# Optimization experiments

Measured on AMD Instinct MI355X. Metric: run time of the kernel, lower is better.

Reference implementation:

```python
import jax, jax.numpy as jnp
import numpy as np

B, T, D, N, K, H = 2, 2048, 2048, 16, 8, 128
WIN = 1024                      # sliding_window_size
SOFT_CAP = 50.0                 # attn_logits_soft_cap
SCALAR = 0.08838834764831845    # query_pre_attn_scalar = head_dim**-0.5
K_MASK = -2.3819763e+38
ROPE_BASE = 10000.0
ROPE_SCALE = 1.0


def apply_rope(x, positions):
    # x: [B, T, heads, H]; positions: [B, T]
    head_dim = x.shape[-1]
    half = head_dim // 2
    timescale = ROPE_BASE ** (2.0 * jnp.arange(half, dtype=jnp.float32) / head_dim)
    sinusoid = positions[..., None].astype(jnp.float32) / timescale / ROPE_SCALE  # [B,T,half]
    sin = jnp.sin(sinusoid)[:, :, None, :]
    cos = jnp.cos(sinusoid)[:, :, None, :]
    first, second = jnp.split(x, 2, axis=-1)
    return jnp.concatenate(
        [first * cos - second * sin, second * cos + first * sin], axis=-1
    ).astype(x.dtype)


def setup_inputs() -> dict:
    key = jax.random.key(0)
    k0, k1, k2, k3 = jax.random.split(key, 4)
    x = jax.random.normal(k0, (B, T, D), jnp.float32)
    wq = jax.random.normal(k1, (N, D, H), jnp.float32) * (D ** -0.5)
    wkv = jax.random.normal(k2, (2, K, D, H), jnp.float32) * (D ** -0.5)
    wo = jax.random.normal(k3, (N, H, D), jnp.float32) * ((N * H) ** -0.5)
    segment_pos = jnp.broadcast_to(jnp.arange(T, dtype=jnp.int32), (B, T))
    attn_mask = jnp.broadcast_to(jnp.tril(jnp.ones((T, T), dtype=bool)), (B, T, T))  # causal
    return {"x": x, "wq": wq, "wkv": wkv, "wo": wo,
            "segment_pos": segment_pos, "attn_mask": attn_mask}


def reference(x, wq, wkv, wo, segment_pos, attn_mask):
    # --- projections ---
    q = jnp.einsum('BTD,NDH->BTNH', x, wq)          # [B,T,N,H]
    kv = jnp.einsum('BTD,CKDH->CBTKH', x, wkv)      # [2,B,T,K,H]
    k_proj, v_proj = kv[0], kv[1]
    # --- RoPE + query scaling ---
    q = apply_rope(q, segment_pos) * SCALAR
    k_proj = apply_rope(k_proj, segment_pos)
    # --- GQA logits ---
    G = N // K
    qg = q.reshape(B, T, K, G, H)
    logits = jnp.einsum('BTKGH,BSKH->BTKGS', qg, k_proj).reshape(B, T, N, T)
    # --- soft cap ---
    logits = jnp.tanh(logits / SOFT_CAP) * SOFT_CAP
    # --- sliding-window mask combined with causal attn_mask ---
    all_ones = jnp.ones(attn_mask.shape, dtype=attn_mask.dtype)
    sliding_mask = jnp.triu(all_ones, -WIN + 1) * jnp.tril(all_ones, WIN - 1)
    mask = sliding_mask * attn_mask                  # [B,T,S]
    padded_logits = jnp.where(mask[:, :, None, :], logits, K_MASK)
    probs = jax.nn.softmax(padded_logits, axis=-1).astype(k_proj.dtype)
    # --- GQA weighted values ---
    encoded = jnp.einsum('BTKGS,BSKH->BTKGH',
                         probs.reshape(B, T, K, G, T), v_proj).reshape(B, T, N, H)
    # --- output projection ---
    return jnp.einsum('BTNH,NHD->BTD', encoded, wo)
```

## Files before the change

kernel.cpp:

```cpp
#include <hip/hip_runtime.h>
#include <hip/hip_bf16.h>
#include <stdint.h>

#define BDIM 2
#define TDIM 2048
#define DDIM 2048
#define NHEADS 16
#define KVH 8
#define HDIM 128
#define WINSZ 1024
#define BT (BDIM*TDIM)
#define NHD (NHEADS*HDIM)
#define QKVC 4096

typedef unsigned short u16;
typedef __attribute__((ext_vector_type(8))) short bf16x8;
typedef __attribute__((ext_vector_type(4))) float f32x4;

__device__ __forceinline__ u16 f2bf(float f) {
  union { float f; unsigned u; } v; v.f = f;
  unsigned r = v.u + 0x7FFFu + ((v.u >> 16) & 1u);
  return (u16)(r >> 16);
}
__device__ __forceinline__ float bf2f(u16 u) {
  union { unsigned u; float f; } v; v.u = ((unsigned)u) << 16;
  return v.f;
}

__device__ __forceinline__ void gl_lds16(const u16* g, u16* l) {
  __builtin_amdgcn_global_load_lds((const __attribute__((address_space(1))) void*)g,
                                   (__attribute__((address_space(3))) void*)l, 16, 0, 0);
}

__global__ __launch_bounds__(256) void k_prep(const float* __restrict__ x, const float* __restrict__ wq,
                                              const float* __restrict__ wkv, const float* __restrict__ wo,
                                              const int* __restrict__ seg,
                                              u16* __restrict__ x_bf, u16* __restrict__ wt_qkv,
                                              u16* __restrict__ wo_t, float2* __restrict__ tab) {
  const int id = blockIdx.x, tid = threadIdx.x;
  if (id < 8192) {
    __shared__ float tl0[32][33];
    int tx = tid & 31, ty = tid >> 5;
    int r0 = (id & 127) * 32, c0 = (id >> 7) * 32;
    #pragma unroll
    for (int i = 0; i < 4; i++) {
      int r = r0 + tx, c = c0 + ty + i*8;
      const float* sp; size_t off;
      if (r < 2048) { sp = wq; off = (size_t)(r >> 7)*262144u + (size_t)(r & 127); }
      else { int j = r - 2048; sp = wkv; off = (size_t)((j >> 10)*8 + ((j >> 7) & 7))*262144u + (size_t)(j & 127); }
      off += (size_t)c * 128u;
      tl0[tx][ty + i*8] = sp[off];
    }
    __syncthreads();
    #pragma unroll
    for (int i = 0; i < 4; i++) {
      int rl = ty + i*8;
      wt_qkv[(size_t)(r0 + rl)*2048u + (size_t)(c0 + tx)] = f2bf(tl0[rl][tx]);
    }
  } else if (id < 16384) {
    int i = (id - 8192)*256 + tid;
    float4 v = ((const float4*)x)[i];
    ushort4 o;
    o.x = f2bf(v.x); o.y = f2bf(v.y); o.z = f2bf(v.z); o.w = f2bf(v.w);
    ((ushort4*)x_bf)[i] = o;
  } else if (id < 20480) {
    __shared__ float tl1[32][33];
    int id3 = id - 16384;
    int tx = tid & 31, ty = tid >> 5;
    int r0 = (id3 & 63) * 32, c0 = (id3 >> 6) * 32;
    #pragma unroll
    for (int i = 0; i < 4; i++) {
      int r = r0 + tx, c = c0 + ty + i*8;
      tl1[tx][ty + i*8] = wo[(size_t)c * 2048u + (size_t)r];
    }
    __syncthreads();
    #pragma unroll
    for (int i = 0; i < 4; i++) {
      int rl = ty + i*8;
      wo_t[(size_t)(r0 + rl)*2048u + (size_t)(c0 + tx)] = f2bf(tl1[rl][tx]);
    }
  } else {
    int bt = (id - 20480)*4 + (tid >> 6);
    int i = tid & 63;
    int pos = seg[bt];
    float inv_ts = exp2f(-(float)i * (13.287712379549449f/64.0f));
    float ang = (float)pos * inv_ts;
    tab[(size_t)bt*64 + i] = make_float2(cosf(ang), sinf(ang));
  }
}

template<int F32OUT>
__global__ __launch_bounds__(256) void k_gemm(const u16* __restrict__ A, const u16* __restrict__ Bt,
                                              void* __restrict__ Cout, int M, int Ncols, int Kdim, int ldc) {
  __shared__ u16 As[128*64];
  __shared__ u16 Bs[128*64];
  const int tid = threadIdx.x, lane = tid & 63, wave = tid >> 6;
  const int m0 = blockIdx.x * 128, n0 = blockIdx.y * 128;
  const int wr = wave >> 1, wc = wave & 1;
  const int l15 = lane & 15, lg = lane >> 4;
  f32x4 acc[4][4] = {};
  for (int kt = 0; kt < Kdim; kt += 64) {
    __syncthreads();
    #pragma unroll
    for (int i = 0; i < 4; i++) {
      int chb = i*256 + wave*64;
      int ch = chb + lane;
      int r = ch >> 3, cc = ch & 7;
      gl_lds16(A + (size_t)(m0 + r)*Kdim + kt + cc*8, As + chb*8);
      gl_lds16(Bt + (size_t)(n0 + r)*Kdim + kt + cc*8, Bs + chb*8);
    }
    __syncthreads();
    #pragma unroll
    for (int ks = 0; ks < 2; ks++) {
      bf16x8 af[4], bf[4];
      int kk = ks*32 + lg*8;
      #pragma unroll
      for (int mt = 0; mt < 4; mt++) af[mt] = *(const bf16x8*)(As + (wr*64 + mt*16 + l15)*64 + kk);
      #pragma unroll
      for (int nt = 0; nt < 4; nt++) bf[nt] = *(const bf16x8*)(Bs + (wc*64 + nt*16 + l15)*64 + kk);
      #pragma unroll
      for (int mt = 0; mt < 4; mt++)
        #pragma unroll
        for (int nt = 0; nt < 4; nt++)
          acc[mt][nt] = __builtin_amdgcn_mfma_f32_16x16x32_bf16(af[mt], bf[nt], acc[mt][nt], 0, 0, 0);
    }
  }
  #pragma unroll
  for (int mt = 0; mt < 4; mt++) {
    int row = m0 + wr*64 + mt*16 + lg*4;
    #pragma unroll
    for (int nt = 0; nt < 4; nt++) {
      int col = n0 + wc*64 + nt*16 + l15;
      #pragma unroll
      for (int j = 0; j < 4; j++) {
        if (F32OUT) ((float*)Cout)[(size_t)(row + j)*ldc + col] = acc[mt][nt][j];
        else        ((u16*)Cout)[(size_t)(row + j)*ldc + col] = f2bf(acc[mt][nt][j]);
      }
    }
  }
}

template<int F32OUT>
__global__ __launch_bounds__(512, 2) void k_gemm8(const u16* __restrict__ A, const u16* __restrict__ Bt,
                                                  void* __restrict__ Cout, int M, int Ncols, int Kdim, int ldc) {
  __shared__ u16 As[2][256*64];
  __shared__ u16 Bs[2][256*64];
  const int tid = threadIdx.x, lane = tid & 63, wave = tid >> 6;
  const int l15 = lane & 15, lg = lane >> 4;
  const int wm = wave >> 2, wn = wave & 3;
  const int gx = M >> 8, gy = Ncols >> 8;
  const int nwg = gx * gy;
  int bid = blockIdx.x;
  int q = nwg >> 3, r = nwg & 7;
  int xcd = bid & 7, idx = bid >> 3;
  int wg = (xcd < r ? xcd*(q+1) : r*(q+1) + (xcd - r)*q) + idx;
  const int m0 = (wg % gx) * 256, n0 = (wg / gx) * 256;

  const int st_r = tid >> 3;
  const int st_c = (tid & 7) ^ (st_r & 7);

  const u16* Ag = A + (size_t)(m0 + st_r)*Kdim + st_c*8;
  const u16* Bg = Bt + (size_t)(n0 + st_r)*Kdim + st_c*8;

  auto stage = [&](int t, int h) {
    int buf = t & 1;
    if (h < 2) {
      const u16* g = Bg + (size_t)(h*128)*Kdim + t*64;
      u16* d = &Bs[buf][h*8192 + wave*512];
      gl_lds16(g, d);
      gl_lds16(g + (size_t)64*Kdim, d + 4096);
    } else {
      int hh = h - 2;
      const u16* g = Ag + (size_t)(hh*128)*Kdim + t*64;
      u16* d = &As[buf][hh*8192 + wave*512];
      gl_lds16(g, d);
      gl_lds16(g + (size_t)64*Kdim, d + 4096);
    }
  };

  const int aBase = (wm*128 + l15) * 128;
  const int bBase = (wn*64 + l15) * 128;
  const int kx0 = ((lg) ^ (l15 & 7)) << 4;
  const int kx1 = ((4 + lg) ^ (l15 & 7)) << 4;

  f32x4 acc[8][4] = {};
  bf16x8 af[4][2], bfr[4][2];

  stage(0,0); stage(0,1); stage(0,2); stage(0,3);
  asm volatile("s_waitcnt vmcnt(4)" ::: "memory");
  stage(1,0); stage(1,1); stage(1,2);
  asm volatile("s_waitcnt vmcnt(6)" ::: "memory");
  __builtin_amdgcn_s_barrier();

  const int NT = Kdim >> 6;

#define MFMA_Q(MS, NS)                                                          \
  { _Pragma("unroll") for (int mf = 0; mf < 4; mf++)                            \
    _Pragma("unroll") for (int nf = 0; nf < 2; nf++) {                          \
      acc[(MS)+mf][(NS)+nf] = __builtin_amdgcn_mfma_f32_16x16x32_bf16(af[mf][0], bfr[(NS)+nf][0], acc[(MS)+mf][(NS)+nf], 0, 0, 0); \
      acc[(MS)+mf][(NS)+nf] = __builtin_amdgcn_mfma_f32_16x16x32_bf16(af[mf][1], bfr[(NS)+nf][1], acc[(MS)+mf][(NS)+nf], 0, 0, 0); \
  } }

  for (int t = 0; t < NT; ++t) {
    const int cur = t & 1;
    const char* Ab = (const char*)&As[cur][0];
    const char* Bb = (const char*)&Bs[cur][0];
    #pragma unroll
    for (int mf = 0; mf < 4; mf++) {
      af[mf][0] = *(const bf16x8*)(Ab + aBase + mf*2048 + kx0);
      af[mf][1] = *(const bf16x8*)(Ab + aBase + mf*2048 + kx1);
    }
    #pragma unroll
    for (int nf = 0; nf < 2; nf++) {
      bfr[nf][0] = *(const bf16x8*)(Bb + bBase + nf*2048 + kx0);
      bfr[nf][1] = *(const bf16x8*)(Bb + bBase + nf*2048 + kx1);
    }
    if (t + 1 < NT) stage(t+1, 3);
    asm volatile("s_waitcnt lgkmcnt(8)" ::: "memory");
    __builtin_amdgcn_s_barrier();
    asm volatile("" ::: "memory");
    __builtin_amdgcn_s_setprio(1);
    MFMA_Q(0, 0)
    __builtin_amdgcn_s_setprio(0);
    __builtin_amdgcn_s_barrier();
    #pragma unroll
    for (int nf = 2; nf < 4; nf++) {
      bfr[nf][0] = *(const bf16x8*)(Bb + bBase + nf*2048 + kx0);
      bfr[nf][1] = *(const bf16x8*)(Bb + bBase + nf*2048 + kx1);
    }
    __builtin_amdgcn_s_barrier();
    asm volatile("" ::: "memory");
    __builtin_amdgcn_s_setprio(1);
    MFMA_Q(0, 2)
    __builtin_amdgcn_s_setprio(0);
    __builtin_amdgcn_s_barrier();
    #pragma unroll
    for (int mf = 0; mf < 4; mf++) {
      af[mf][0] = *(const bf16x8*)(Ab + aBase + 8192 + mf*2048 + kx0);
      af[mf][1] = *(const bf16x8*)(Ab + aBase + 8192 + mf*2048 + kx1);
    }
    if (t + 2 < NT) { stage(t+2, 0); stage(t+2, 1); }
    __builtin_amdgcn_s_barrier();
    asm volatile("" ::: "memory");
    __builtin_amdgcn_s_setprio(1);
    MFMA_Q(4, 2)
    __builtin_amdgcn_s_setprio(0);
    __builtin_amdgcn_s_barrier();
    if (t + 2 < NT) {
      stage(t+2, 2);
      asm volatile("s_waitcnt vmcnt(6)" ::: "memory");
    } else if (t + 1 < NT) {
      asm volatile("s_waitcnt vmcnt(0)" ::: "memory");
    }
    __builtin_amdgcn_s_barrier();
    asm volatile("" ::: "memory");
    __builtin_amdgcn_s_setprio(1);
    MFMA_Q(4, 0)
    __builtin_amdgcn_s_setprio(0);
    __builtin_amdgcn_s_barrier();
  }
#undef MFMA_Q

  #pragma unroll
  for (int mf = 0; mf < 8; mf++) {
    int row = m0 + wm*128 + mf*16 + lg*4;
    #pragma unroll
    for (int nf = 0; nf < 4; nf++) {
      int col = n0 + wn*64 + nf*16 + l15;
      #pragma unroll
      for (int j = 0; j < 4; j++) {
        if (F32OUT) ((float*)Cout)[(size_t)(row + j)*ldc + col] = acc[mf][nf][j];
        else        ((u16*)Cout)[(size_t)(row + j)*ldc + col] = f2bf(acc[mf][nf][j]);
      }
    }
  }
}

__global__ __launch_bounds__(256) void k_ropevt(u16* __restrict__ qkv, const float2* __restrict__ tab,
                                                u16* __restrict__ vT) {
  const int id = blockIdx.x, tid = threadIdx.x;
  if (id < 4096) {
    if (tid < 192) {
      const int bt = id;
      const int h = tid >> 3, g = tid & 7;
      const int col0 = (h < 16 ? h*128 : 2048 + (h - 16)*128) + g*8;
      const float sc = (h < 16) ? 0.08838834764831845f : 1.0f;
      u16* row = qkv + (size_t)bt*QKVC;
      bf16x8 v1 = *(const bf16x8*)(row + col0);
      bf16x8 v2 = *(const bf16x8*)(row + col0 + 64);
      const float4* t4 = (const float4*)(tab + (size_t)bt*64 + g*8);
      bf16x8 r1, r2;
      #pragma unroll
      for (int i = 0; i < 4; i++) {
        float4 cs2 = t4[i];
        float f0 = bf2f((u16)v1[2*i]),   s0 = bf2f((u16)v2[2*i]);
        float f1 = bf2f((u16)v1[2*i+1]), s1 = bf2f((u16)v2[2*i+1]);
        r1[2*i]   = (short)f2bf((f0*cs2.x - s0*cs2.y)*sc);
        r2[2*i]   = (short)f2bf((s0*cs2.x + f0*cs2.y)*sc);
        r1[2*i+1] = (short)f2bf((f1*cs2.z - s1*cs2.w)*sc);
        r2[2*i+1] = (short)f2bf((s1*cs2.z + f1*cs2.w)*sc);
      }
      *(bf16x8*)(row + col0) = r1;
      *(bf16x8*)(row + col0 + 64) = r2;
    }
  } else {
    __shared__ u16 tl[32][33];
    const int id2 = id - 4096;
    const int tx = tid & 31, ty = tid >> 5;
    const int t0 = (id2 & 63)*32, h0 = ((id2 >> 6) & 3)*32, bk = id2 >> 8;
    const u16* src = qkv + (size_t)(bk >> 3)*TDIM*QKVC + 3072 + (bk & 7)*HDIM;
    #pragma unroll
    for (int i = 0; i < 4; i++)
      tl[ty + i*8][tx] = src[(size_t)(t0 + ty + i*8)*QKVC + h0 + tx];
    __syncthreads();
    u16* dst = vT + (size_t)bk*HDIM*TDIM;
    #pragma unroll
    for (int i = 0; i < 4; i++)
      dst[(size_t)(h0 + ty + i*8)*TDIM + t0 + tx] = tl[tx][ty + i*8];
  }
}

__device__ __forceinline__ void stage_tiles(const u16* __restrict__ kg, const u16* __restrict__ vg,
                                            u16* ldsK, u16* ldsV, int tid) {
  const int w = tid >> 6;
  const int rK = tid >> 4, cK = tid & 15;
  u16* dK = ldsK + w*512;
  gl_lds16(kg + (size_t)rK*QKVC + ((cK ^ (rK & 15)) << 3), dK);
  gl_lds16(kg + (size_t)(rK + 32)*QKVC + ((cK ^ ((rK + 32) & 15)) << 3), dK + 4096);
  const int rV = tid >> 3, cV = tid & 7;
  u16* dV = ldsV + w*512;
  gl_lds16(vg + (size_t)rV*TDIM + ((cV ^ (rV & 7)) << 3), dV);
  gl_lds16(vg + (size_t)(rV + 64)*TDIM + ((cV ^ ((rV + 64) & 7)) << 3), dV + 4096);
}

__global__ __launch_bounds__(512, 4) void k_attn(const u16* __restrict__ qkv, const u16* __restrict__ vT,
                                                 u16* __restrict__ enc) {
  __shared__ u16 Kb[2][64*128];
  __shared__ u16 Vb[2][128*64];
  __shared__ u16 Pl[8][16*64];
  const int tid = threadIdx.x;
  const int lane = tid & 63, wave = tid >> 6;
  const int l15 = lane & 15, lg = lane >> 4;
  const int wg = blockIdx.x;
  const int lin = (wg & 7)*64 + (wg >> 3);
  const int qt = lin & 31, kvh = (lin >> 5) & 7, b = lin >> 8;
  const int n = kvh*2 + (wave >> 2);
  const int t0 = qt * 64;
  const int lo_row = t0 + (wave & 3)*16, hi_row = lo_row + 15;

  bf16x8 qf[4];
  {
    const u16* qb = qkv + (size_t)(b*TDIM + lo_row + l15)*QKVC + n*HDIM + lg*8;
    #pragma unroll
    for (int ks = 0; ks < 4; ks++) qf[ks] = *(const bf16x8*)(qb + ks*32);
  }
  f32x4 o[8] = {};
  f32x4 o_l = {};
  const short one_bf = (short)0x3F80;
  const bf16x8 ones = {one_bf, one_bf, one_bf, one_bf, one_bf, one_bf, one_bf, one_bf};

  const u16* kgb = qkv + (size_t)(b*TDIM)*QKVC + 2048 + kvh*HDIM;
  const u16* vgb = vT + (size_t)(b*KVH + kvh)*HDIM*TDIM;

  const float L0 = 1.4426950408889634f;
  const float L1 = -1.9235933878519513e-4f;
  const float L2 = 3.0777094205631089e-8f;
  const float BIAS = -72.13475204444817f;

  const int s_begin = (t0 >= 1024) ? (t0 - 1024) : 0;
  stage_tiles(kgb + (size_t)s_begin*QKVC, vgb + s_begin, Kb[0], Vb[0], tid);
  int cur = 0;
  for (int s0 = s_begin; s0 <= t0; s0 += 64) {
    if (s0 + 64 <= t0) {
      stage_tiles(kgb + (size_t)(s0 + 64)*QKVC, vgb + (s0 + 64), Kb[cur ^ 1], Vb[cur ^ 1], tid);
      asm volatile("s_waitcnt vmcnt(4)" ::: "memory");
    } else {
      asm volatile("s_waitcnt vmcnt(0)" ::: "memory");
    }
    __builtin_amdgcn_s_barrier();
    __builtin_amdgcn_sched_barrier(0);

    const u16* Kc = Kb[cur];
    const u16* Vc = Vb[cur];
    f32x4 sc4[4];
    #pragma unroll
    for (int c = 0; c < 4; c++) {
      const int cLo = s0 + c*16;
      bool anyLive = (cLo <= hi_row) && (cLo + 15 >= lo_row - (WINSZ - 1));
      bool full    = (cLo + 15 <= lo_row) && (cLo >= hi_row - (WINSZ - 1));
      f32x4 a = {0.f, 0.f, 0.f, 0.f};
      if (anyLive) {
        int krow = c*16 + l15;
        __builtin_amdgcn_s_setprio(1);
        #pragma unroll
        for (int ks = 0; ks < 4; ks++) {
          bf16x8 kf = *(const bf16x8*)(Kc + krow*128 + (((ks*4 + lg) ^ l15) << 3));
          a = __builtin_amdgcn_mfma_f32_16x16x32_bf16(qf[ks], kf, a, 0, 0, 0);
        }
        __builtin_amdgcn_s_setprio(0);
        if (full) {
          #pragma unroll
          for (int j = 0; j < 4; j++) {
            float z = a[j];
            float u = z*z;
            float tt = __builtin_fmaf(u, __builtin_fmaf(u, L2, L1), L0);
            a[j] = exp2f(__builtin_fmaf(z, tt, BIAS));
          }
        } else {
          #pragma unroll
          for (int j = 0; j < 4; j++) {
            int scol = cLo + l15;
            int trow = lo_row + lg*4 + j;
            float z = a[j];
            float u = z*z;
            float tt = __builtin_fmaf(u, __builtin_fmaf(u, L2, L1), L0);
            float p = exp2f(__builtin_fmaf(z, tt, BIAS));
            bool ok = (scol <= trow) && (scol >= trow - (WINSZ - 1));
            a[j] = ok ? p : 0.f;
          }
        }
      }
      sc4[c] = a;
    }
    #pragma unroll
    for (int c = 0; c < 4; c++)
      #pragma unroll
      for (int j = 0; j < 4; j++) {
        int prow = lg*4 + j, pcol = c*16 + l15;
        int off = prow*128 + pcol*2; off ^= (prow & 7) << 4;
        __hip_bfloat16 hb = __float2bfloat16(sc4[c][j]);
        *(u16*)((char*)(&Pl[wave][0]) + off) = *reinterpret_cast<u16*>(&hb);
      }
    __builtin_amdgcn_s_setprio(1);
    #pragma unroll
    for (int ks = 0; ks < 2; ks++) {
      int roff = l15*128 + ks*64 + lg*16; roff ^= (l15 & 7) << 4;
      bf16x8 pf = *(const bf16x8*)((char*)(&Pl[wave][0]) + roff);
      o_l = __builtin_amdgcn_mfma_f32_16x16x32_bf16(pf, ones, o_l, 0, 0, 0);
      #pragma unroll
      for (int ct = 0; ct < 8; ct++) {
        int vrow = ct*16 + l15;
        bf16x8 vf = *(const bf16x8*)(Vc + vrow*64 + (((ks*4 + lg) ^ (l15 & 7)) << 3));
        o[ct] = __builtin_amdgcn_mfma_f32_16x16x32_bf16(pf, vf, o[ct], 0, 0, 0);
      }
    }
    __builtin_amdgcn_s_setprio(0);
    __builtin_amdgcn_s_barrier();
    cur ^= 1;
  }
  #pragma unroll
  for (int j = 0; j < 4; j++) {
    float inv = __fdividef(1.f, o_l[j]);
    int row = lo_row + lg*4 + j;
    u16* eb = enc + (size_t)(b*TDIM + row)*NHD + n*HDIM;
    #pragma unroll
    for (int ct = 0; ct < 8; ct++)
      eb[ct*16 + l15] = f2bf(o[ct][j] * inv);
  }
}

extern "C" void kernel_launch(void* const* d_in, const int* in_sizes, int n_in,
                              void* d_out, int out_size, void* d_ws, size_t ws_size,
                              hipStream_t stream) {
  const float* x   = (const float*)d_in[0];
  const float* wq  = (const float*)d_in[1];
  const float* wkv = (const float*)d_in[2];
  const float* wo  = (const float*)d_in[3];
  const int*   seg = (const int*)d_in[4];
  float* out = (float*)d_out;

  char* ws = (char*)d_ws;
  u16*    x_bf   = (u16*)(ws);
  u16*    wt_qkv = (u16*)(ws + (16u << 20));
  u16*    qkv    = (u16*)(ws + (32u << 20));
  u16*    vT     = (u16*)(ws + (64u << 20));
  u16*    enc    = (u16*)(ws + (72u << 20));
  u16*    wo_t   = (u16*)(ws + (88u << 20));
  float2* tab    = (float2*)(ws + (96u << 20));

  k_prep<<<dim3(21504), 256, 0, stream>>>(x, wq, wkv, wo, seg, x_bf, wt_qkv, wo_t, tab);
  k_gemm8<0><<<dim3((BT/256)*(QKVC/256)), 512, 0, stream>>>(x_bf, wt_qkv, qkv, BT, QKVC, DDIM, QKVC);
  k_ropevt<<<dim3(8192), 256, 0, stream>>>(qkv, tab, vT);
  k_attn<<<dim3(512), 512, 0, stream>>>(qkv, vT, enc);
  k_gemm<1><<<dim3(BT/128, DDIM/128), 256, 0, stream>>>(enc, wo_t, out, BT, DDIM, NHD, DDIM);
}
```

Before: 204.2 us.

## Fuse Q RoPE into attention, single-buffer K/V, remap output GEMM blocks per XCD

Query RoPE and scaling move from the separate rope kernel into the attention kernel's Q-fragment load, so that kernel now only rotates K and transposes V. Attention drops K/V double buffering for a single buffer with synchronous loads, and raises the occupancy hint from 4 to 6 blocks per CU. The tanh soft-cap polynomial loses its highest-order term, and the output GEMM launches a 1D grid remapped so neighbouring tiles land on the same XCD. The changes trade load/compute overlap for lower LDS use and higher occupancy, and the shorter polynomial slightly changes numerics.

```diff
diff --git a/kernel.cpp b/kernel.cpp
--- a/kernel.cpp
+++ b/kernel.cpp
@@ -1,5 +1,4 @@
 #include <hip/hip_runtime.h>
-#include <hip/hip_bf16.h>
 #include <stdint.h>
 
 #define BDIM 2
@@ -95,7 +94,10 @@
   __shared__ u16 As[128*64];
   __shared__ u16 Bs[128*64];
   const int tid = threadIdx.x, lane = tid & 63, wave = tid >> 6;
-  const int m0 = blockIdx.x * 128, n0 = blockIdx.y * 128;
+  const int bid = blockIdx.x;
+  const int xcd = bid & 7, idx = bid >> 3;
+  const int m0 = (((xcd & 3) << 3) + (idx & 7)) * 128;
+  const int n0 = (((xcd >> 2) << 3) + (idx >> 3)) * 128;
   const int wr = wave >> 1, wc = wave & 1;
   const int l15 = lane & 15, lg = lane >> 4;
   f32x4 acc[4][4] = {};
@@ -276,33 +278,23 @@
   }
 }
 
-__global__ __launch_bounds__(256) void k_ropevt(u16* __restrict__ qkv, const float2* __restrict__ tab,
-                                                u16* __restrict__ vT) {
+__global__ __launch_bounds__(256) void k_kvt(u16* __restrict__ qkv, const float2* __restrict__ tab,
+                                             u16* __restrict__ vT) {
   const int id = blockIdx.x, tid = threadIdx.x;
   if (id < 4096) {
-    if (tid < 192) {
-      const int bt = id;
-      const int h = tid >> 3, g = tid & 7;
-      const int col0 = (h < 16 ? h*128 : 2048 + (h - 16)*128) + g*8;
-      const float sc = (h < 16) ? 0.08838834764831845f : 1.0f;
-      u16* row = qkv + (size_t)bt*QKVC;
-      bf16x8 v1 = *(const bf16x8*)(row + col0);
-      bf16x8 v2 = *(const bf16x8*)(row + col0 + 64);
-      const float4* t4 = (const float4*)(tab + (size_t)bt*64 + g*8);
-      bf16x8 r1, r2;
-      #pragma unroll
-      for (int i = 0; i < 4; i++) {
-        float4 cs2 = t4[i];
-        float f0 = bf2f((u16)v1[2*i]),   s0 = bf2f((u16)v2[2*i]);
-        float f1 = bf2f((u16)v1[2*i+1]), s1 = bf2f((u16)v2[2*i+1]);
-        r1[2*i]   = (short)f2bf((f0*cs2.x - s0*cs2.y)*sc);
-        r2[2*i]   = (short)f2bf((s0*cs2.x + f0*cs2.y)*sc);
-        r1[2*i+1] = (short)f2bf((f1*cs2.z - s1*cs2.w)*sc);
-        r2[2*i+1] = (short)f2bf((s1*cs2.z + f1*cs2.w)*sc);
-      }
-      *(bf16x8*)(row + col0) = r1;
-      *(bf16x8*)(row + col0 + 64) = r2;
-    }
+    const int bt = id;
+    const int kh = tid >> 5, ii = (tid & 31) * 2;
+    u16* row = qkv + (size_t)bt*QKVC + 2048 + kh*128 + ii;
+    const float2 c0 = tab[(size_t)bt*64 + ii];
+    const float2 c1 = tab[(size_t)bt*64 + ii + 1];
+    unsigned fu = *(const unsigned*)row;
+    unsigned su = *(const unsigned*)(row + 64);
+    float f0 = bf2f((u16)(fu & 0xffff)), f1 = bf2f((u16)(fu >> 16));
+    float s0 = bf2f((u16)(su & 0xffff)), s1 = bf2f((u16)(su >> 16));
+    unsigned ro = (unsigned)f2bf(f0*c0.x - s0*c0.y) | ((unsigned)f2bf(f1*c1.x - s1*c1.y) << 16);
+    unsigned rs = (unsigned)f2bf(s0*c0.x + f0*c0.y) | ((unsigned)f2bf(s1*c1.x + f1*c1.y) << 16);
+    *(unsigned*)row = ro;
+    *(unsigned*)(row + 64) = rs;
   } else {
     __shared__ u16 tl[32][33];
     const int id2 = id - 4096;
@@ -333,10 +325,10 @@
   gl_lds16(vg + (size_t)(rV + 64)*TDIM + ((cV ^ ((rV + 64) & 7)) << 3), dV + 4096);
 }
 
-__global__ __launch_bounds__(512, 4) void k_attn(const u16* __restrict__ qkv, const u16* __restrict__ vT,
-                                                 u16* __restrict__ enc) {
-  __shared__ u16 Kb[2][64*128];
-  __shared__ u16 Vb[2][128*64];
+__global__ __launch_bounds__(512, 6) void k_attn(const u16* __restrict__ qkv, const u16* __restrict__ vT,
+                                                 const float2* __restrict__ tab, u16* __restrict__ enc) {
+  __shared__ u16 Kb[64*128];
+  __shared__ u16 Vb[128*64];
   __shared__ u16 Pl[8][16*64];
   const int tid = threadIdx.x;
   const int lane = tid & 63, wave = tid >> 6;
@@ -350,9 +342,21 @@
 
   bf16x8 qf[4];
   {
-    const u16* qb = qkv + (size_t)(b*TDIM + lo_row + l15)*QKVC + n*HDIM + lg*8;
+    const int qrow = b*TDIM + lo_row + l15;
+    const u16* qb = qkv + (size_t)qrow*QKVC + n*HDIM + lg*8;
     #pragma unroll
     for (int ks = 0; ks < 4; ks++) qf[ks] = *(const bf16x8*)(qb + ks*32);
+    const float2* trow = tab + (size_t)qrow*64 + lg*8;
+    const float SC = 0.08838834764831845f;
+    #pragma unroll
+    for (int ks = 0; ks < 2; ks++)
+      #pragma unroll
+      for (int e = 0; e < 8; e++) {
+        float2 cs = trow[ks*32 + e];
+        float f = bf2f((u16)qf[ks][e]), s = bf2f((u16)qf[ks+2][e]);
+        qf[ks][e]   = (short)f2bf((f*cs.x - s*cs.y) * SC);
+        qf[ks+2][e] = (short)f2bf((s*cs.x + f*cs.y) * SC);
+      }
   }
   f32x4 o[8] = {};
   f32x4 o_l = {};
@@ -363,25 +367,16 @@
   const u16* vgb = vT + (size_t)(b*KVH + kvh)*HDIM*TDIM;
 
   const float L0 = 1.4426950408889634f;
-  const float L1 = -1.9235933878519513e-4f;
-  const float L2 = 3.0777094205631089e-8f;
+  const float C1L = -1.9235933878519513e-4f;
   const float BIAS = -72.13475204444817f;
 
   const int s_begin = (t0 >= 1024) ? (t0 - 1024) : 0;
-  stage_tiles(kgb + (size_t)s_begin*QKVC, vgb + s_begin, Kb[0], Vb[0], tid);
-  int cur = 0;
+  stage_tiles(kgb + (size_t)s_begin*QKVC, vgb + s_begin, Kb, Vb, tid);
+  asm volatile("s_waitcnt vmcnt(0)" ::: "memory");
+  __builtin_amdgcn_s_barrier();
+  __builtin_amdgcn_sched_barrier(0);
+
   for (int s0 = s_begin; s0 <= t0; s0 += 64) {
-    if (s0 + 64 <= t0) {
-      stage_tiles(kgb + (size_t)(s0 + 64)*QKVC, vgb + (s0 + 64), Kb[cur ^ 1], Vb[cur ^ 1], tid);
-      asm volatile("s_waitcnt vmcnt(4)" ::: "memory");
-    } else {
-      asm volatile("s_waitcnt vmcnt(0)" ::: "memory");
-    }
-    __builtin_amdgcn_s_barrier();
-    __builtin_amdgcn_sched_barrier(0);
-
-    const u16* Kc = Kb[cur];
-    const u16* Vc = Vb[cur];
     f32x4 sc4[4];
     #pragma unroll
     for (int c = 0; c < 4; c++) {
@@ -394,7 +389,7 @@
         __builtin_amdgcn_s_setprio(1);
         #pragma unroll
         for (int ks = 0; ks < 4; ks++) {
-          bf16x8 kf = *(const bf16x8*)(Kc + krow*128 + (((ks*4 + lg) ^ l15) << 3));
+          bf16x8 kf = *(const bf16x8*)(Kb + krow*128 + (((ks*4 + lg) ^ l15) << 3));
           a = __builtin_amdgcn_mfma_f32_16x16x32_bf16(qf[ks], kf, a, 0, 0, 0);
         }
         __builtin_amdgcn_s_setprio(0);
@@ -402,20 +397,18 @@
           #pragma unroll
           for (int j = 0; j < 4; j++) {
             float z = a[j];
-            float u = z*z;
-            float tt = __builtin_fmaf(u, __builtin_fmaf(u, L2, L1), L0);
+            float tt = __builtin_fmaf(z*z, C1L, L0);
             a[j] = exp2f(__builtin_fmaf(z, tt, BIAS));
           }
         } else {
           #pragma unroll
           for (int j = 0; j < 4; j++) {
             int scol = cLo + l15;
-            int trow = lo_row + lg*4 + j;
+            int trow2 = lo_row + lg*4 + j;
             float z = a[j];
-            float u = z*z;
-            float tt = __builtin_fmaf(u, __builtin_fmaf(u, L2, L1), L0);
+            float tt = __builtin_fmaf(z*z, C1L, L0);
             float p = exp2f(__builtin_fmaf(z, tt, BIAS));
-            bool ok = (scol <= trow) && (scol >= trow - (WINSZ - 1));
+            bool ok = (scol <= trow2) && (scol >= trow2 - (WINSZ - 1));
             a[j] = ok ? p : 0.f;
           }
         }
@@ -428,8 +421,7 @@
       for (int j = 0; j < 4; j++) {
         int prow = lg*4 + j, pcol = c*16 + l15;
         int off = prow*128 + pcol*2; off ^= (prow & 7) << 4;
-        __hip_bfloat16 hb = __float2bfloat16(sc4[c][j]);
-        *(u16*)((char*)(&Pl[wave][0]) + off) = *reinterpret_cast<u16*>(&hb);
+        *(u16*)((char*)(&Pl[wave][0]) + off) = f2bf(sc4[c][j]);
       }
     __builtin_amdgcn_s_setprio(1);
     #pragma unroll
@@ -440,13 +432,18 @@
       #pragma unroll
       for (int ct = 0; ct < 8; ct++) {
         int vrow = ct*16 + l15;
-        bf16x8 vf = *(const bf16x8*)(Vc + vrow*64 + (((ks*4 + lg) ^ (l15 & 7)) << 3));
+        bf16x8 vf = *(const bf16x8*)(Vb + vrow*64 + (((ks*4 + lg) ^ (l15 & 7)) << 3));
         o[ct] = __builtin_amdgcn_mfma_f32_16x16x32_bf16(pf, vf, o[ct], 0, 0, 0);
       }
     }
     __builtin_amdgcn_s_setprio(0);
     __builtin_amdgcn_s_barrier();
-    cur ^= 1;
+    if (s0 + 64 <= t0) {
+      stage_tiles(kgb + (size_t)(s0 + 64)*QKVC, vgb + (s0 + 64), Kb, Vb, tid);
+      asm volatile("s_waitcnt vmcnt(0)" ::: "memory");
+    }
+    __builtin_amdgcn_s_barrier();
+    __builtin_amdgcn_sched_barrier(0);
   }
   #pragma unroll
   for (int j = 0; j < 4; j++) {
@@ -480,7 +477,7 @@
 
   k_prep<<<dim3(21504), 256, 0, stream>>>(x, wq, wkv, wo, seg, x_bf, wt_qkv, wo_t, tab);
   k_gemm8<0><<<dim3((BT/256)*(QKVC/256)), 512, 0, stream>>>(x_bf, wt_qkv, qkv, BT, QKVC, DDIM, QKVC);
-  k_ropevt<<<dim3(8192), 256, 0, stream>>>(qkv, tab, vT);
-  k_attn<<<dim3(512), 512, 0, stream>>>(qkv, vT, enc);
-  k_gemm<1><<<dim3(BT/128, DDIM/128), 256, 0, stream>>>(enc, wo_t, out, BT, DDIM, NHD, DDIM);
-}
+  k_kvt<<<dim3(8192), 256, 0, stream>>>(qkv, tab, vT);
+  k_attn<<<dim3(512), 512, 0, stream>>>(qkv, vT, tab, enc);
+  k_gemm<1><<<dim3(512), 256, 0, stream>>>(enc, wo_t, out, BT, DDIM, NHD, DDIM);
+}
```

Result: slower. 407.6 us (+99.6%).
